# Kernel optimization log

Measured on AMD Instinct MI355X. Metric: run time of the kernel, lower is better.

## Reference

```python
import jax, jax.numpy as jnp
import numpy as np

E, TOPK, C = 8, 2, 1  # num_local_experts, num_experts_per_tok, num_channels
BS, L, D, F = 8, 1024, 1024, 4096


def setup_inputs() -> dict:
    key = jax.random.key(0)
    ks = jax.random.split(key, 5)
    s = lambda fan_in: 1.0 / np.sqrt(fan_in)
    return {
        "hidden_states": jax.random.normal(ks[0], (BS, L, D), jnp.float32),
        # nn.Linear weight layout [out, in]
        "router_w": jax.random.normal(ks[1], (E, D * C), jnp.float32) * s(D * C),
        "w1": jax.random.normal(ks[2], (E, F, D), jnp.float32) * s(D),
        "w2": jax.random.normal(ks[3], (E, D, F), jnp.float32) * s(F),
        "w3": jax.random.normal(ks[4], (E, F, D), jnp.float32) * s(D),
    }


def _forward(hidden_states, router_w, w1, w2, w3):
    bs, seq, d = hidden_states.shape  # 3D path -> c = 1
    c = C
    h = hidden_states.reshape(bs, seq, c * d)  # [bs, L, c*d]
    # router: per-position logits, then mean over sequence (sentence-level routing)
    router_logits = jnp.einsum('blf,ef->ble', h, router_w).mean(axis=1)  # [bs, E]
    router_probs = jax.nn.softmax(router_logits, axis=-1)
    topk_w, topk_idx = jax.lax.top_k(router_probs, TOPK)  # [bs, TOPK]

    # dense all-expert SwiGLU MLP on every token (as in the original)
    x = h.reshape(bs, seq, c, d)
    outs = []
    for e in range(E):  # fixed small expert count
        up = jnp.einsum('blcd,fd->blcf', x, w1[e])
        gate = jnp.einsum('blcd,fd->blcf', x, w3[e])
        y = jnp.einsum('blcf,df->blcd', jax.nn.silu(up) * gate, w2[e])
        outs.append(y.reshape(bs, seq, c * d))
    expert_outputs = jnp.stack(outs, axis=1)  # [bs, E, L, c*d]

    # Faithful replication of torch.gather(dim=1) with index [bs,L,TOPK,h]:
    # out[b,l,j,:] = expert_outputs[b, topk_idx[b,j], j, :]  (independent of l)
    bi = jnp.arange(bs)[:, None]
    ji = jnp.arange(TOPK)[None, :]
    sel = expert_outputs[bi, topk_idx, ji]  # [bs, TOPK, c*d]
    combined = (sel * topk_w[..., None]).sum(axis=1)  # [bs, c*d]
    out = jnp.broadcast_to(combined[:, None, :], (bs, seq, c * d))
    out = out.reshape(bs, c, seq, d)
    return out, router_logits


def reference(hidden_states, router_w, w1, w2, w3):
    return _forward(hidden_states, router_w, w1, w2, w3)
```

## Files before the change

### kernel.cpp

```cpp
#include <hip/hip_runtime.h>
#include <math.h>

#define BS 8
#define SEQ 1024
#define DIM 1024
#define FF 4096
#define NE 8
#define TOPK 2
#define NSLOT (BS*TOPK)
#define MAXM 8
#define NCHUNK 64

#define WS_PARTIAL 0
#define WS_LOGITS  (WS_PARTIAL + BS*NCHUNK*DIM)
#define WS_SELW    (WS_LOGITS + BS*NE)
#define WS_SELE    (WS_SELW + NSLOT)
#define WS_ACT     (WS_SELE + NSLOT)
#define WS_Y       (WS_ACT + NSLOT*FF)

__device__ __forceinline__ float dot4(float4 a, float4 b) {
    return a.x*b.x + a.y*b.y + a.z*b.z + a.w*b.w;
}

__global__ __launch_bounds__(256) void kmean(const float4* __restrict__ h4,
                                             float4* __restrict__ part4) {
    const int c = blockIdx.x, b = blockIdx.y, t = threadIdx.x;
    const int LPER = SEQ / NCHUNK;
    const float4* p = h4 + ((size_t)b * SEQ + (size_t)c * LPER) * (DIM/4) + t;
    float4 a = make_float4(0.f, 0.f, 0.f, 0.f);
    #pragma unroll
    for (int i = 0; i < LPER; ++i) {
        float4 v = p[(size_t)i * (DIM/4)];
        a.x += v.x; a.y += v.y; a.z += v.z; a.w += v.w;
    }
    part4[((size_t)(b * NCHUNK + c)) * (DIM/4) + t] = a;
}

__global__ __launch_bounds__(256) void krouter(const float4* __restrict__ part4,
                                               const float4* __restrict__ rw4,
                                               float* __restrict__ logits_ws,
                                               float* __restrict__ out_logits) {
    const int b = blockIdx.x, t = threadIdx.x;
    const float4* p = part4 + (size_t)b * NCHUNK * (DIM/4) + t;
    float4 s = make_float4(0.f, 0.f, 0.f, 0.f);
    #pragma unroll 4
    for (int c = 0; c < NCHUNK; ++c) {
        float4 v = p[(size_t)c * (DIM/4)];
        s.x += v.x; s.y += v.y; s.z += v.z; s.w += v.w;
    }
    const float inv = 1.0f / (float)SEQ;
    s.x *= inv; s.y *= inv; s.z *= inv; s.w *= inv;

    __shared__ float red[4];
    const int wave = t >> 6, lane = t & 63;
    for (int e = 0; e < NE; ++e) {
        float4 w = rw4[(size_t)e * (DIM/4) + t];
        float pd = dot4(s, w);
        #pragma unroll
        for (int o = 32; o; o >>= 1) pd += __shfl_xor(pd, o);
        if (lane == 0) red[wave] = pd;
        __syncthreads();
        if (t == 0) {
            float l = red[0] + red[1] + red[2] + red[3];
            logits_ws[b * NE + e] = l;
            out_logits[b * NE + e] = l;
        }
        __syncthreads();
    }
}

__global__ void ktopk(const float* __restrict__ logits,
                      float* __restrict__ selw, int* __restrict__ sele) {
    const int b = threadIdx.x;
    if (b >= BS) return;
    float l[NE];
    float mx = -1e30f;
    #pragma unroll
    for (int e = 0; e < NE; ++e) { l[e] = logits[b * NE + e]; mx = fmaxf(mx, l[e]); }
    float s = 0.f;
    #pragma unroll
    for (int e = 0; e < NE; ++e) { l[e] = expf(l[e] - mx); s += l[e]; }
    const float invs = 1.f / s;
    float v1 = -1.f, v2 = -1.f; int e1 = -1, e2 = -1;
    #pragma unroll
    for (int e = 0; e < NE; ++e) {
        float pe = l[e] * invs;
        if (pe > v1)      { v2 = v1; e2 = e1; v1 = pe; e1 = e; }
        else if (pe > v2) { v2 = pe; e2 = e; }
    }
    selw[b * 2 + 0] = v1; sele[b * 2 + 0] = e1;
    selw[b * 2 + 1] = v2; sele[b * 2 + 1] = e2;
}

#define ROWS_UG 32
__global__ __launch_bounds__(256) void kupgate(const float* __restrict__ h,
                                               const float4* __restrict__ w1_4,
                                               const float4* __restrict__ w3_4,
                                               const int* __restrict__ sele,
                                               float* __restrict__ act) {
    const int e = blockIdx.y, tile = blockIdx.x, t = threadIdx.x;
    __shared__ int slots_s[MAXM];
    __shared__ int ms;
    __shared__ __align__(16) float x_s[MAXM][DIM];
    if (t == 0) {
        int m = 0;
        for (int s = 0; s < NSLOT; ++s) if (sele[s] == e) slots_s[m++] = s;
        ms = m;
    }
    __syncthreads();
    const int m = ms;
    if (m == 0) return;

    for (int ti = 0; ti < m; ++ti) {
        int s = slots_s[ti];
        int b = s >> 1, j = s & 1;
        const float4* src = (const float4*)(h + ((size_t)b * SEQ + j) * DIM);
        ((float4*)&x_s[ti][0])[t] = src[t];
    }
    __syncthreads();

    const int wave = t >> 6, lane = t & 63;
    for (int k = 0; k < ROWS_UG / 4; ++k) {
        const int row = tile * ROWS_UG + wave * (ROWS_UG / 4) + k;
        float up[MAXM], gt[MAXM];
        #pragma unroll
        for (int i = 0; i < MAXM; ++i) { up[i] = 0.f; gt[i] = 0.f; }
        const float4* w1r = w1_4 + ((size_t)e * FF + row) * (DIM/4) + lane;
        const float4* w3r = w3_4 + ((size_t)e * FF + row) * (DIM/4) + lane;
        #pragma unroll
        for (int it = 0; it < 4; ++it) {
            float4 a = w1r[it * 64];
            float4 c = w3r[it * 64];
            #pragma unroll
            for (int ti = 0; ti < MAXM; ++ti) {
                if (ti < m) {
                    float4 x = ((const float4*)&x_s[ti][0])[it * 64 + lane];
                    up[ti] += dot4(a, x);
                    gt[ti] += dot4(c, x);
                }
            }
        }
        #pragma unroll
        for (int ti = 0; ti < MAXM; ++ti) {
            if (ti < m) {
                float u = up[ti], g = gt[ti];
                #pragma unroll
                for (int o = 32; o; o >>= 1) { u += __shfl_xor(u, o); g += __shfl_xor(g, o); }
                if (lane == 0) {
                    float av = (u / (1.f + expf(-u))) * g;
                    act[(size_t)slots_s[ti] * FF + row] = av;
                }
            }
        }
    }
}

#define ROWS_DN 8
__global__ __launch_bounds__(256) void kdown(const float4* __restrict__ w2_4,
                                             const float* __restrict__ act,
                                             const int* __restrict__ sele,
                                             const float* __restrict__ selw,
                                             float* __restrict__ y) {
    const int e = blockIdx.y, tile = blockIdx.x, t = threadIdx.x;
    __shared__ int slots_s[MAXM];
    __shared__ int ms;
    __shared__ __align__(16) float a_s[MAXM][1024];
    if (t == 0) {
        int m = 0;
        for (int s = 0; s < NSLOT; ++s) if (sele[s] == e) slots_s[m++] = s;
        ms = m;
    }
    __syncthreads();
    const int m = ms;
    if (m == 0) return;

    const int wave = t >> 6, lane = t & 63;
    float acc[2][MAXM];
    #pragma unroll
    for (int r = 0; r < 2; ++r)
        #pragma unroll
        for (int i = 0; i < MAXM; ++i) acc[r][i] = 0.f;

    for (int kc = 0; kc < 4; ++kc) {
        __syncthreads();
        for (int ti = 0; ti < m; ++ti) {
            int s = slots_s[ti];
            ((float4*)&a_s[ti][0])[t] =
                ((const float4*)(act + (size_t)s * FF + kc * 1024))[t];
        }
        __syncthreads();
        #pragma unroll
        for (int r = 0; r < 2; ++r) {
            const int row = tile * ROWS_DN + wave * 2 + r;
            const float4* w2r = w2_4 + ((size_t)e * DIM + row) * (FF/4) + kc * 256 + lane;
            #pragma unroll
            for (int it = 0; it < 4; ++it) {
                float4 w = w2r[it * 64];
                #pragma unroll
                for (int ti = 0; ti < MAXM; ++ti) {
                    if (ti < m) {
                        float4 x = ((const float4*)&a_s[ti][0])[it * 64 + lane];
                        acc[r][ti] += dot4(w, x);
                    }
                }
            }
        }
    }
    #pragma unroll
    for (int r = 0; r < 2; ++r) {
        const int row = tile * ROWS_DN + wave * 2 + r;
        #pragma unroll
        for (int ti = 0; ti < MAXM; ++ti) {
            if (ti < m) {
                float v = acc[r][ti];
                #pragma unroll
                for (int o = 32; o; o >>= 1) v += __shfl_xor(v, o);
                if (lane == 0) {
                    int s = slots_s[ti];
                    y[(size_t)s * DIM + row] = selw[s] * v;
                }
            }
        }
    }
}

__global__ __launch_bounds__(256) void kbcast(const float4* __restrict__ y4,
                                              float4* __restrict__ out4) {
    const int b = blockIdx.y, lg = blockIdx.x, t = threadIdx.x;
    float4 y0 = y4[(size_t)(2 * b) * (DIM/4) + t];
    float4 y1 = y4[(size_t)(2 * b + 1) * (DIM/4) + t];
    float4 c = make_float4(y0.x + y1.x, y0.y + y1.y, y0.z + y1.z, y0.w + y1.w);
    size_t base = ((size_t)b * SEQ + (size_t)lg * 8) * (DIM/4) + t;
    #pragma unroll
    for (int i = 0; i < 8; ++i) out4[base + (size_t)i * (DIM/4)] = c;
}

extern "C" void kernel_launch(void* const* d_in, const int* in_sizes, int n_in,
                              void* d_out, int out_size, void* d_ws, size_t ws_size,
                              hipStream_t stream) {
    const float* h  = (const float*)d_in[0];
    const float* rw = (const float*)d_in[1];
    const float* w1 = (const float*)d_in[2];
    const float* w2 = (const float*)d_in[3];
    const float* w3 = (const float*)d_in[4];
    float* out = (float*)d_out;
    float* ws  = (float*)d_ws;

    float* part   = ws + WS_PARTIAL;
    float* logits = ws + WS_LOGITS;
    float* selw   = ws + WS_SELW;
    int*   sele   = (int*)(ws + WS_SELE);
    float* act    = ws + WS_ACT;
    float* y      = ws + WS_Y;
    float* out_logits = out + (size_t)BS * SEQ * DIM;

    kmean  <<<dim3(NCHUNK, BS), 256, 0, stream>>>((const float4*)h, (float4*)part);
    krouter<<<BS, 256, 0, stream>>>((const float4*)part, (const float4*)rw, logits, out_logits);
    ktopk  <<<1, 64, 0, stream>>>(logits, selw, sele);
    kupgate<<<dim3(FF / ROWS_UG, NE), 256, 0, stream>>>(h, (const float4*)w1, (const float4*)w3, sele, act);
    kdown  <<<dim3(DIM / ROWS_DN, NE), 256, 0, stream>>>((const float4*)w2, act, sele, selw, y);
    kbcast <<<dim3(SEQ / 8, BS), 256, 0, stream>>>((const float4*)y, (float4*)out);
}
```

Measured before the change: 128.7 us.

## Fuse top-k into router and specialize expert GEMV kernels by slot count

The softmax/top-k step moves into the router kernel, which removes one launch. The up/gate and down kernels drop the LDS staging and syncthreads and read activations directly from global memory, relying on L1/L2 cache. Each expert block now builds its slot list with a bitmask and dispatches to a template instantiation for the exact token count, so no predicated wasted iterations run. Each row is now computed by a 16-lane group instead of a full 64-lane wave, and the down tile grows to 16 rows, which shortens shuffle reductions at the cost of more global loads of x.

New measurement: 134.2 us. +4.3%, slower.

```diff
diff --git a/kernel.cpp b/kernel.cpp
--- a/kernel.cpp
+++ b/kernel.cpp
@@ -10,6 +10,8 @@
 #define NSLOT (BS*TOPK)
 #define MAXM 8
 #define NCHUNK 64
+#define UG_TILE 32
+#define DN_TILE 16
 
 #define WS_PARTIAL 0
 #define WS_LOGITS  (WS_PARTIAL + BS*NCHUNK*DIM)
@@ -38,8 +40,9 @@
 
 __global__ __launch_bounds__(256) void krouter(const float4* __restrict__ part4,
                                                const float4* __restrict__ rw4,
-                                               float* __restrict__ logits_ws,
-                                               float* __restrict__ out_logits) {
+                                               float* __restrict__ out_logits,
+                                               float* __restrict__ selw,
+                                               int* __restrict__ sele) {
     const int b = blockIdx.x, t = threadIdx.x;
     const float4* p = part4 + (size_t)b * NCHUNK * (DIM/4) + t;
     float4 s = make_float4(0.f, 0.f, 0.f, 0.f);
@@ -52,6 +55,7 @@
     s.x *= inv; s.y *= inv; s.z *= inv; s.w *= inv;
 
     __shared__ float red[4];
+    __shared__ float lg[NE];
     const int wave = t >> 6, lane = t & 63;
     for (int e = 0; e < NE; ++e) {
         float4 w = rw4[(size_t)e * (DIM/4) + t];
@@ -62,165 +66,162 @@
         __syncthreads();
         if (t == 0) {
             float l = red[0] + red[1] + red[2] + red[3];
-            logits_ws[b * NE + e] = l;
+            lg[e] = l;
             out_logits[b * NE + e] = l;
         }
         __syncthreads();
     }
-}
-
-__global__ void ktopk(const float* __restrict__ logits,
-                      float* __restrict__ selw, int* __restrict__ sele) {
-    const int b = threadIdx.x;
-    if (b >= BS) return;
-    float l[NE];
-    float mx = -1e30f;
-    #pragma unroll
-    for (int e = 0; e < NE; ++e) { l[e] = logits[b * NE + e]; mx = fmaxf(mx, l[e]); }
-    float s = 0.f;
-    #pragma unroll
-    for (int e = 0; e < NE; ++e) { l[e] = expf(l[e] - mx); s += l[e]; }
-    const float invs = 1.f / s;
-    float v1 = -1.f, v2 = -1.f; int e1 = -1, e2 = -1;
-    #pragma unroll
-    for (int e = 0; e < NE; ++e) {
-        float pe = l[e] * invs;
-        if (pe > v1)      { v2 = v1; e2 = e1; v1 = pe; e1 = e; }
-        else if (pe > v2) { v2 = pe; e2 = e; }
-    }
-    selw[b * 2 + 0] = v1; sele[b * 2 + 0] = e1;
-    selw[b * 2 + 1] = v2; sele[b * 2 + 1] = e2;
-}
-
-#define ROWS_UG 32
-__global__ __launch_bounds__(256) void kupgate(const float* __restrict__ h,
+    if (t == 0) {
+        float l[NE];
+        float mx = -1e30f;
+        #pragma unroll
+        for (int e = 0; e < NE; ++e) { l[e] = lg[e]; mx = fmaxf(mx, l[e]); }
+        float sum = 0.f;
+        #pragma unroll
+        for (int e = 0; e < NE; ++e) { l[e] = expf(l[e] - mx); sum += l[e]; }
+        const float invs = 1.f / sum;
+        float v1 = -1.f, v2 = -1.f; int e1 = -1, e2 = -1;
+        #pragma unroll
+        for (int e = 0; e < NE; ++e) {
+            float pe = l[e] * invs;
+            if (pe > v1)      { v2 = v1; e2 = e1; v1 = pe; e1 = e; }
+            else if (pe > v2) { v2 = pe; e2 = e; }
+        }
+        selw[b * 2 + 0] = v1; sele[b * 2 + 0] = e1;
+        selw[b * 2 + 1] = v2; sele[b * 2 + 1] = e2;
+    }
+}
+
+__device__ __forceinline__ int build_slots(const int* __restrict__ sele, int e, int* slot) {
+    unsigned mask = 0;
+    #pragma unroll
+    for (int s = 0; s < NSLOT; ++s) mask |= (sele[s] == e) ? (1u << s) : 0u;
+    const int m = __popc(mask);
+    unsigned mm = mask;
+    #pragma unroll
+    for (int ti = 0; ti < MAXM; ++ti) { slot[ti] = __ffs(mm) - 1; mm &= mm - 1; }
+    return m;
+}
+
+template<int M>
+__device__ __forceinline__ void upgate_work(const float4* __restrict__ h4,
+                                            const float4* __restrict__ w1_4,
+                                            const float4* __restrict__ w3_4,
+                                            float* __restrict__ act,
+                                            const int* slot, int e, int tile, int t) {
+    const int wave = t >> 6, g = (t >> 4) & 3, l = t & 15;
+    const float4* xp[M];
+    #pragma unroll
+    for (int ti = 0; ti < M; ++ti) {
+        const int s = slot[ti];
+        xp[ti] = h4 + ((size_t)((s >> 1) * SEQ + (s & 1))) * (DIM/4) + l;
+    }
+    #pragma unroll
+    for (int k = 0; k < 2; ++k) {
+        const int row = tile * UG_TILE + wave * 8 + k * 4 + g;
+        const float4* w1r = w1_4 + ((size_t)e * FF + row) * (DIM/4) + l;
+        const float4* w3r = w3_4 + ((size_t)e * FF + row) * (DIM/4) + l;
+        float up[M], gt[M];
+        #pragma unroll
+        for (int ti = 0; ti < M; ++ti) { up[ti] = 0.f; gt[ti] = 0.f; }
+        #pragma unroll
+        for (int it = 0; it < 16; ++it) {
+            float4 a = w1r[it * 16];
+            float4 c = w3r[it * 16];
+            #pragma unroll
+            for (int ti = 0; ti < M; ++ti) {
+                float4 x = xp[ti][it * 16];
+                up[ti] += dot4(a, x);
+                gt[ti] += dot4(c, x);
+            }
+        }
+        #pragma unroll
+        for (int ti = 0; ti < M; ++ti) {
+            float u = up[ti], gg = gt[ti];
+            #pragma unroll
+            for (int o = 8; o; o >>= 1) { u += __shfl_xor(u, o); gg += __shfl_xor(gg, o); }
+            if (l == 0) {
+                act[(size_t)slot[ti] * FF + row] = (u / (1.f + expf(-u))) * gg;
+            }
+        }
+    }
+}
+
+__global__ __launch_bounds__(256) void kupgate(const float4* __restrict__ h4,
                                                const float4* __restrict__ w1_4,
                                                const float4* __restrict__ w3_4,
                                                const int* __restrict__ sele,
                                                float* __restrict__ act) {
     const int e = blockIdx.y, tile = blockIdx.x, t = threadIdx.x;
-    __shared__ int slots_s[MAXM];
-    __shared__ int ms;
-    __shared__ __align__(16) float x_s[MAXM][DIM];
-    if (t == 0) {
-        int m = 0;
-        for (int s = 0; s < NSLOT; ++s) if (sele[s] == e) slots_s[m++] = s;
-        ms = m;
-    }
-    __syncthreads();
-    const int m = ms;
+    int slot[MAXM];
+    const int m = build_slots(sele, e, slot);
     if (m == 0) return;
-
-    for (int ti = 0; ti < m; ++ti) {
-        int s = slots_s[ti];
-        int b = s >> 1, j = s & 1;
-        const float4* src = (const float4*)(h + ((size_t)b * SEQ + j) * DIM);
-        ((float4*)&x_s[ti][0])[t] = src[t];
-    }
-    __syncthreads();
-
-    const int wave = t >> 6, lane = t & 63;
-    for (int k = 0; k < ROWS_UG / 4; ++k) {
-        const int row = tile * ROWS_UG + wave * (ROWS_UG / 4) + k;
-        float up[MAXM], gt[MAXM];
-        #pragma unroll
-        for (int i = 0; i < MAXM; ++i) { up[i] = 0.f; gt[i] = 0.f; }
-        const float4* w1r = w1_4 + ((size_t)e * FF + row) * (DIM/4) + lane;
-        const float4* w3r = w3_4 + ((size_t)e * FF + row) * (DIM/4) + lane;
-        #pragma unroll
-        for (int it = 0; it < 4; ++it) {
-            float4 a = w1r[it * 64];
-            float4 c = w3r[it * 64];
-            #pragma unroll
-            for (int ti = 0; ti < MAXM; ++ti) {
-                if (ti < m) {
-                    float4 x = ((const float4*)&x_s[ti][0])[it * 64 + lane];
-                    up[ti] += dot4(a, x);
-                    gt[ti] += dot4(c, x);
-                }
-            }
-        }
-        #pragma unroll
-        for (int ti = 0; ti < MAXM; ++ti) {
-            if (ti < m) {
-                float u = up[ti], g = gt[ti];
-                #pragma unroll
-                for (int o = 32; o; o >>= 1) { u += __shfl_xor(u, o); g += __shfl_xor(g, o); }
-                if (lane == 0) {
-                    float av = (u / (1.f + expf(-u))) * g;
-                    act[(size_t)slots_s[ti] * FF + row] = av;
-                }
-            }
-        }
-    }
-}
-
-#define ROWS_DN 8
+    switch (m) {
+        case 1: upgate_work<1>(h4, w1_4, w3_4, act, slot, e, tile, t); break;
+        case 2: upgate_work<2>(h4, w1_4, w3_4, act, slot, e, tile, t); break;
+        case 3: upgate_work<3>(h4, w1_4, w3_4, act, slot, e, tile, t); break;
+        case 4: upgate_work<4>(h4, w1_4, w3_4, act, slot, e, tile, t); break;
+        case 5: upgate_work<5>(h4, w1_4, w3_4, act, slot, e, tile, t); break;
+        case 6: upgate_work<6>(h4, w1_4, w3_4, act, slot, e, tile, t); break;
+        case 7: upgate_work<7>(h4, w1_4, w3_4, act, slot, e, tile, t); break;
+        default: upgate_work<8>(h4, w1_4, w3_4, act, slot, e, tile, t); break;
+    }
+}
+
+template<int M>
+__device__ __forceinline__ void down_work(const float4* __restrict__ w2_4,
+                                          const float4* __restrict__ act4,
+                                          const float* __restrict__ selw,
+                                          float* __restrict__ y,
+                                          const int* slot, int e, int tile, int t) {
+    const int wave = t >> 6, g = (t >> 4) & 3, l = t & 15;
+    const float4* ap[M];
+    float sw[M];
+    #pragma unroll
+    for (int ti = 0; ti < M; ++ti) {
+        ap[ti] = act4 + (size_t)slot[ti] * (FF/4) + l;
+        sw[ti] = selw[slot[ti]];
+    }
+    const int row = tile * DN_TILE + wave * 4 + g;
+    const float4* w2r = w2_4 + ((size_t)e * DIM + row) * (FF/4) + l;
+    float acc[M];
+    #pragma unroll
+    for (int ti = 0; ti < M; ++ti) acc[ti] = 0.f;
+    #pragma unroll 16
+    for (int it = 0; it < 64; ++it) {
+        float4 w = w2r[it * 16];
+        #pragma unroll
+        for (int ti = 0; ti < M; ++ti) {
+            acc[ti] += dot4(w, ap[ti][it * 16]);
+        }
+    }
+    #pragma unroll
+    for (int ti = 0; ti < M; ++ti) {
+        float v = acc[ti];
+        #pragma unroll
+        for (int o = 8; o; o >>= 1) v += __shfl_xor(v, o);
+        if (l == 0) y[(size_t)slot[ti] * DIM + row] = sw[ti] * v;
+    }
+}
+
 __global__ __launch_bounds__(256) void kdown(const float4* __restrict__ w2_4,
-                                             const float* __restrict__ act,
+                                             const float4* __restrict__ act4,
                                              const int* __restrict__ sele,
                                              const float* __restrict__ selw,
                                              float* __restrict__ y) {
     const int e = blockIdx.y, tile = blockIdx.x, t = threadIdx.x;
-    __shared__ int slots_s[MAXM];
-    __shared__ int ms;
-    __shared__ __align__(16) float a_s[MAXM][1024];
-    if (t == 0) {
-        int m = 0;
-        for (int s = 0; s < NSLOT; ++s) if (sele[s] == e) slots_s[m++] = s;
-        ms = m;
-    }
-    __syncthreads();
-    const int m = ms;
+    int slot[MAXM];
+    const int m = build_slots(sele, e, slot);
     if (m == 0) return;
-
-    const int wave = t >> 6, lane = t & 63;
-    float acc[2][MAXM];
-    #pragma unroll
-    for (int r = 0; r < 2; ++r)
-        #pragma unroll
-        for (int i = 0; i < MAXM; ++i) acc[r][i] = 0.f;
-
-    for (int kc = 0; kc < 4; ++kc) {
-        __syncthreads();
-        for (int ti = 0; ti < m; ++ti) {
-            int s = slots_s[ti];
-            ((float4*)&a_s[ti][0])[t] =
-                ((const float4*)(act + (size_t)s * FF + kc * 1024))[t];
-        }
-        __syncthreads();
-        #pragma unroll
-        for (int r = 0; r < 2; ++r) {
-            const int row = tile * ROWS_DN + wave * 2 + r;
-            const float4* w2r = w2_4 + ((size_t)e * DIM + row) * (FF/4) + kc * 256 + lane;
-            #pragma unroll
-            for (int it = 0; it < 4; ++it) {
-                float4 w = w2r[it * 64];
-                #pragma unroll
-                for (int ti = 0; ti < MAXM; ++ti) {
-                    if (ti < m) {
-                        float4 x = ((const float4*)&a_s[ti][0])[it * 64 + lane];
-                        acc[r][ti] += dot4(w, x);
-                    }
-                }
-            }
-        }
-    }
-    #pragma unroll
-    for (int r = 0; r < 2; ++r) {
-        const int row = tile * ROWS_DN + wave * 2 + r;
-        #pragma unroll
-        for (int ti = 0; ti < MAXM; ++ti) {
-            if (ti < m) {
-                float v = acc[r][ti];
-                #pragma unroll
-                for (int o = 32; o; o >>= 1) v += __shfl_xor(v, o);
-                if (lane == 0) {
-                    int s = slots_s[ti];
-                    y[(size_t)s * DIM + row] = selw[s] * v;
-                }
-            }
-        }
+    switch (m) {
+        case 1: down_work<1>(w2_4, act4, selw, y, slot, e, tile, t); break;
+        case 2: down_work<2>(w2_4, act4, selw, y, slot, e, tile, t); break;
+        case 3: down_work<3>(w2_4, act4, selw, y, slot, e, tile, t); break;
+        case 4: down_work<4>(w2_4, act4, selw, y, slot, e, tile, t); break;
+        case 5: down_work<5>(w2_4, act4, selw, y, slot, e, tile, t); break;
+        case 6: down_work<6>(w2_4, act4, selw, y, slot, e, tile, t); break;
+        case 7: down_work<7>(w2_4, act4, selw, y, slot, e, tile, t); break;
+        default: down_work<8>(w2_4, act4, selw, y, slot, e, tile, t); break;
     }
 }
 
@@ -247,7 +248,6 @@
     float* ws  = (float*)d_ws;
 
     float* part   = ws + WS_PARTIAL;
-    float* logits = ws + WS_LOGITS;
     float* selw   = ws + WS_SELW;
     int*   sele   = (int*)(ws + WS_SELE);
     float* act    = ws + WS_ACT;
@@ -255,9 +255,10 @@
     float* out_logits = out + (size_t)BS * SEQ * DIM;
 
     kmean  <<<dim3(NCHUNK, BS), 256, 0, stream>>>((const float4*)h, (float4*)part);
-    krouter<<<BS, 256, 0, stream>>>((const float4*)part, (const float4*)rw, logits, out_logits);
-    ktopk  <<<1, 64, 0, stream>>>(logits, selw, sele);
-    kupgate<<<dim3(FF / ROWS_UG, NE), 256, 0, stream>>>(h, (const float4*)w1, (const float4*)w3, sele, act);
-    kdown  <<<dim3(DIM / ROWS_DN, NE), 256, 0, stream>>>((const float4*)w2, act, sele, selw, y);
+    krouter<<<BS, 256, 0, stream>>>((const float4*)part, (const float4*)rw, out_logits, selw, sele);
+    kupgate<<<dim3(FF / UG_TILE, NE), 256, 0, stream>>>((const float4*)h, (const float4*)w1,
+                                                        (const float4*)w3, sele, act);
+    kdown  <<<dim3(DIM / DN_TILE, NE), 256, 0, stream>>>((const float4*)w2, (const float4*)act,
+                                                         sele, selw, y);
     kbcast <<<dim3(SEQ / 8, BS), 256, 0, stream>>>((const float4*)y, (float4*)out);
 }
```
